# Kernel tuning notes

Hardware: AMD Instinct MI355X
Metric: run time of the kernel (lower is better)

The kernel has to match this reference:

```python
import jax, jax.numpy as jnp
import numpy as np

EMBED = 768
HEADS = 12
HEAD_DIM = EMBED // HEADS

def setup_inputs() -> dict:
    key = jax.random.key(0)
    k1, k2, k3, k4 = jax.random.split(key, 4)
    x = jax.random.normal(k1, (8, 1024, EMBED), dtype=jnp.float32)
    # qkv Linear (no bias per qkv_bias=False); proj Linear with bias
    w_qkv = jax.random.normal(k2, (EMBED, 3 * EMBED), dtype=jnp.float32) * 0.02
    w_proj = jax.random.normal(k3, (EMBED, EMBED), dtype=jnp.float32) * 0.02
    b_proj = jax.random.normal(k4, (EMBED,), dtype=jnp.float32) * 0.02
    return {"x": x, "w_qkv": w_qkv, "w_proj": w_proj, "b_proj": b_proj}

def reference(x, w_qkv, w_proj, b_proj):
    b, n, e = x.shape
    h, d = HEADS, HEAD_DIM
    scale = d ** (-0.5)
    qkv = x @ w_qkv                                    # [b, n, 3*e]
    qkv = qkv.reshape(b, n, 3, h, d)                   # (qkv h d) split order
    q, k, v = (jnp.transpose(qkv[:, :, i], (0, 2, 1, 3)) for i in range(3))  # [b,h,n,d]
    dots = jnp.einsum('bhid,bhjd->bhij', q, k) * scale
    attn = jax.nn.softmax(dots, axis=-1)               # dropout p=0 -> identity
    out = jnp.einsum('bhij,bhjd->bhid', attn, v)       # [b,h,n,d]
    out = jnp.transpose(out, (0, 2, 1, 3)).reshape(b, n, e)
    return out @ w_proj + b_proj
```

## Files before the change

kernel.cpp:

```cpp
#include <hip/hip_runtime.h>

typedef _Float16 f16;
typedef _Float16 half8 __attribute__((ext_vector_type(8)));
typedef _Float16 half4v __attribute__((ext_vector_type(4)));
typedef __fp16 fp16x2 __attribute__((ext_vector_type(2)));
typedef float f32x4 __attribute__((ext_vector_type(4)));
typedef float f32x16 __attribute__((ext_vector_type(16)));
typedef unsigned uint4v __attribute__((ext_vector_type(4)));

#define MFMA16(a,b,c) __builtin_amdgcn_mfma_f32_16x16x32_f16((a),(b),(c),0,0,0)
#define MFMA32(a,b,c) __builtin_amdgcn_mfma_f32_32x32x16_f16((a),(b),(c),0,0,0)

__device__ __forceinline__ void gload_lds16(const f16* g, f16* l) {
    __builtin_amdgcn_global_load_lds(
        (const __attribute__((address_space(1))) unsigned int*)g,
        (__attribute__((address_space(3))) unsigned int*)l, 16, 0, 0);
}

__device__ __forceinline__ void plswap(unsigned &a, unsigned &b) {
    asm volatile("v_permlane32_swap_b32 %0, %1" : "+v"(a), "+v"(b));
}

__device__ __forceinline__ unsigned pk2(float a, float b) {
    return __builtin_bit_cast(unsigned, __builtin_amdgcn_cvt_pkrtz(a, b));
}

__device__ __forceinline__ float fexp2(float x) {
#if __has_builtin(__builtin_amdgcn_exp2f)
    return __builtin_amdgcn_exp2f(x);
#else
    return exp2f(x);
#endif
}

__device__ __forceinline__ float xswap32(float x, int hi) {
    unsigned a = __builtin_bit_cast(unsigned, x), b = a;
    asm volatile("v_permlane32_swap_b32 %0, %1" : "+v"(a), "+v"(b));
    return __builtin_bit_cast(float, hi ? a : b);
}

__global__ void prep_kernel(const float* __restrict__ x, f16* __restrict__ x_h,
                            const float* __restrict__ w_qkv, f16* __restrict__ w_qkv_t,
                            const float* __restrict__ w_proj, f16* __restrict__ w_proj_t)
{
    __shared__ f16 tile[32][33];
    const int bidx = blockIdx.x;
    if (bidx < 6144) {
        int i = bidx * 256 + threadIdx.x;
        float4 v = ((const float4*)x)[i];
        half4v h;
        h.x = (f16)v.x; h.y = (f16)v.y; h.z = (f16)v.z; h.w = (f16)v.w;
        ((half4v*)x_h)[i] = h;
        return;
    }
    const float* in;  f16* out;  int N, idx;
    if (bidx < 6144 + 1728) { idx = bidx - 6144; in = w_qkv;  out = w_qkv_t;  N = 2304; }
    else                    { idx = bidx - 7872; in = w_proj; out = w_proj_t; N = 768;  }
    const int K = 768;
    int n0 = (idx % (N / 32)) * 32, k0 = (idx / (N / 32)) * 32;
    int tx = threadIdx.x & 31, ty = threadIdx.x >> 5;
    for (int r = ty; r < 32; r += 8)
        tile[r][tx] = (f16)in[(size_t)(k0 + r) * N + (n0 + tx)];
    __syncthreads();
    for (int r = ty; r < 32; r += 8)
        out[(size_t)(n0 + r) * K + (k0 + tx)] = tile[tx][r];
}

__global__ __launch_bounds__(256, 5)
void gemm_qkv(const f16* __restrict__ A, const f16* __restrict__ Bt,
              f16* __restrict__ qbuf, f16* __restrict__ kbuf, f16* __restrict__ vtbuf)
{
    constexpr int K = 768;
    constexpr int NX = 18;
    constexpr int NWG = NX * 64;
    __shared__ __align__(16) char smem[32768];
    f16* As = (f16*)smem;
    f16* Bs = (f16*)(smem + 16384);
    const int tid  = threadIdx.x;
    const int lane = tid & 63, wave = tid >> 6;
    const int wm = wave >> 1, wn = wave & 1;
    const int l15 = lane & 15, l4 = lane >> 4;

    const int bid = blockIdx.x;
    const int swz = (bid & 7) * (NWG / 8) + (bid >> 3);
    const int m0 = (swz / NX) * 128, n0 = (swz % NX) * 128;

    const int srow  = lane >> 2;
    const int sslot = lane & 3;

    f32x4 acc[4][4] = {};

    #define GSTAGE(buf, kt) do {                                                     \
        _Pragma("unroll")                                                            \
        for (int i = 0; i < 2; ++i) {                                                \
            int rbase = i * 64 + wave * 16;                                          \
            int row = rbase + srow;                                                  \
            gload_lds16(A  + (size_t)(m0 + row) * K + (kt) + sslot * 8, &As[(buf) * 4096 + rbase * 32]); \
            gload_lds16(Bt + (size_t)(n0 + row) * K + (kt) + sslot * 8, &Bs[(buf) * 4096 + rbase * 32]); \
        }                                                                            \
    } while (0)

    GSTAGE(0, 0);
    __syncthreads();

    for (int t = 0; t < 24; ++t) {
        const int cur = t & 1;
        if (t < 23) GSTAGE(cur ^ 1, (t + 1) * 32);
        half8 af[4], bf[4];
        #pragma unroll
        for (int mi = 0; mi < 4; mi++) af[mi] = *(const half8*)&As[cur*4096 + (wm*64 + mi*16 + l15) * 32 + l4*8];
        #pragma unroll
        for (int ni = 0; ni < 4; ni++) bf[ni] = *(const half8*)&Bs[cur*4096 + (wn*64 + ni*16 + l15) * 32 + l4*8];
        #pragma unroll
        for (int mi = 0; mi < 4; mi++)
            #pragma unroll
            for (int ni = 0; ni < 4; ni++)
                acc[mi][ni] = MFMA16(af[mi], bf[ni], acc[mi][ni]);
        __syncthreads();
    }
    #undef GSTAGE

    const int t3 = n0 / 768;
    const int bb = m0 >> 10;
    const int mo = m0 & 1023;
    const int h0 = (n0 - t3 * 768) >> 6;

    if (t3 < 2) {
        f16* sC = (f16*)smem;
        f16* outb = (t3 == 0) ? qbuf : kbuf;
        #pragma unroll
        for (int hh = 0; hh < 2; hh++) {
            if (wm == hh) {
                #pragma unroll
                for (int mi = 0; mi < 4; mi++)
                    #pragma unroll
                    for (int ni = 0; ni < 4; ni++)
                        #pragma unroll
                        for (int r = 0; r < 4; r++) {
                            int row = mi*16 + l4*4 + r;
                            int col = wn*64 + ni*16 + l15;
                            sC[row * 136 + col] = (f16)acc[mi][ni][r];
                        }
            }
            __syncthreads();
            #pragma unroll
            for (int hc = 0; hc < 2; hc++) {
                f16* base = outb + ((size_t)(bb * 12 + h0 + hc) * 1024 + mo + hh * 64) * 64;
                #pragma unroll
                for (int i = 0; i < 2; i++) {
                    int row = i * 32 + (tid >> 3);
                    int cc  = (tid & 7) * 8;
                    half8 v = *(const half8*)&sC[row * 136 + hc * 64 + cc];
                    *(half8*)(base + row * 64 + cc) = v;
                }
            }
            __syncthreads();
        }
    } else {
        f16* sC = (f16*)smem;
        #pragma unroll
        for (int hh = 0; hh < 2; hh++) {
            if (wn == hh) {
                #pragma unroll
                for (int mi = 0; mi < 4; mi++)
                    #pragma unroll
                    for (int ni = 0; ni < 4; ni++) {
                        int row0 = wm*64 + mi*16 + l4*4;
                        int col  = ni*16 + l15;
                        half4v pk;
                        #pragma unroll
                        for (int r = 0; r < 4; r++) pk[r] = (f16)acc[mi][ni][r];
                        *(half4v*)&sC[col * 136 + row0] = pk;
                    }
            }
            __syncthreads();
            #pragma unroll
            for (int i = 0; i < 4; i++) {
                int col = i * 16 + (tid >> 4);
                int rc  = (tid & 15) * 8;
                half8 v = *(const half8*)&sC[col * 136 + rc];
                int colg = hh * 64 + col;
                int head = h0 + (colg >> 6), dd = colg & 63;
                *(half8*)(vtbuf + ((size_t)(bb * 12 + head) * 64 + dd) * 1024 + mo + rc) = v;
            }
            __syncthreads();
        }
    }
}

__global__ __launch_bounds__(256, 3)
void gemm_proj(const f16* __restrict__ A, const f16* __restrict__ Bt,
               float* __restrict__ out, const float* __restrict__ bias)
{
    constexpr int K = 768;
    constexpr int NX = 6;
    constexpr int NWG = NX * 64;
    __shared__ __align__(16) char smem[49152];
    f16* As = (f16*)smem;
    f16* Bs = (f16*)(smem + 24576);
    const int tid  = threadIdx.x;
    const int lane = tid & 63, wave = tid >> 6;
    const int wm = wave >> 1, wn = wave & 1;
    const int l15 = lane & 15, l4 = lane >> 4;

    const int bid = blockIdx.x;
    const int swz = (bid & 7) * (NWG / 8) + (bid >> 3);
    const int m0 = (swz / NX) * 128, n0 = (swz % NX) * 128;

    const int srow  = lane >> 2;
    const int sslot = lane & 3;

    f32x4 acc[4][4] = {};

    #define GSTAGE(buf, kt) do {                                                     \
        _Pragma("unroll")                                                            \
        for (int i = 0; i < 2; ++i) {                                                \
            int rbase = i * 64 + wave * 16;                                          \
            int row = rbase + srow;                                                  \
            gload_lds16(A  + (size_t)(m0 + row) * K + (kt) + sslot * 8, &As[(buf) * 4096 + rbase * 32]); \
            gload_lds16(Bt + (size_t)(n0 + row) * K + (kt) + sslot * 8, &Bs[(buf) * 4096 + rbase * 32]); \
        }                                                                            \
    } while (0)

    GSTAGE(0, 0);
    GSTAGE(1, 32);

    int cur = 0;
    for (int t = 0; t < 24; ++t) {
        if (t < 23) asm volatile("s_waitcnt vmcnt(4)" ::: "memory");
        else        asm volatile("s_waitcnt vmcnt(0)" ::: "memory");
        __builtin_amdgcn_s_barrier();
        if (t < 22) {
            int nb = cur + 2; if (nb >= 3) nb -= 3;
            GSTAGE(nb, (t + 2) * 32);
        }
        half8 af[4], bf[4];
        #pragma unroll
        for (int mi = 0; mi < 4; mi++) af[mi] = *(const half8*)&As[cur*4096 + (wm*64 + mi*16 + l15) * 32 + l4*8];
        #pragma unroll
        for (int ni = 0; ni < 4; ni++) bf[ni] = *(const half8*)&Bs[cur*4096 + (wn*64 + ni*16 + l15) * 32 + l4*8];
        #pragma unroll
        for (int mi = 0; mi < 4; mi++)
            #pragma unroll
            for (int ni = 0; ni < 4; ni++)
                acc[mi][ni] = MFMA16(af[mi], bf[ni], acc[mi][ni]);
        if (++cur >= 3) cur = 0;
    }
    #undef GSTAGE

    #pragma unroll
    for (int mi = 0; mi < 4; mi++)
        #pragma unroll
        for (int ni = 0; ni < 4; ni++)
            #pragma unroll
            for (int r = 0; r < 4; r++) {
                int gm = m0 + wm*64 + mi*16 + l4*4 + r;
                int gn = n0 + wn*64 + ni*16 + l15;
                out[(size_t)gm * 768 + gn] = acc[mi][ni][r] + bias[gn];
            }
}

__global__ __launch_bounds__(256, 3)
void attn_kernel(const f16* __restrict__ qbuf, const f16* __restrict__ kbuf,
                 const f16* __restrict__ vtbuf, f16* __restrict__ obuf)
{
    __shared__ __align__(16) f16 Ks[3][4096];
    __shared__ __align__(16) f16 Vs[3][4096];
    const int tid = threadIdx.x;
    const int lane = tid & 63, wave = tid >> 6;
    const int bh = blockIdx.x;
    const int b = bh / 12, h = bh % 12;
    const int q0 = blockIdx.y * 128 + wave * 32;
    const int l31 = lane & 31, hi = lane >> 5;
    const int sw0 = (l31 & 7) << 4;

    const f16* Q  = qbuf  + (size_t)bh * 65536;
    const f16* Kp = kbuf  + (size_t)bh * 65536;
    const f16* Vt = vtbuf + (size_t)bh * 65536;

    const f16 slh = (f16)(0.125f * 1.44269504089f);
    half8 aq[4];
    #pragma unroll
    for (int c = 0; c < 4; c++) {
        aq[c] = *(const half8*)&Q[(size_t)(q0 + l31) * 64 + c * 16 + hi * 8];
        #pragma unroll
        for (int j = 0; j < 8; j++) aq[c][j] *= slh;
    }

    const int srow8 = lane >> 3;
    const int c16   = (lane & 7) ^ srow8;

    f32x16 o0 = {}, o1 = {};
    float lrq = 0.f, mrq = 0.f, stale = 0.f;

    #define STAGE(buf, kv) do {                                                     \
        _Pragma("unroll")                                                           \
        for (int i = 0; i < 2; ++i) {                                               \
            int rbase = wave * 16 + i * 8;                                          \
            int rl = rbase + srow8;                                                 \
            gload_lds16(Kp + (size_t)((kv) + rl) * 64 + c16 * 8, &Ks[buf][rbase * 64]); \
            gload_lds16(Vt + (size_t)rl * 1024 + (kv) + c16 * 8, &Vs[buf][rbase * 64]); \
        }                                                                           \
    } while (0)

    #define QKISSUE(dst0, dst1, kb, minit) do {                                     \
        _Pragma("unroll")                                                           \
        for (int j = 0; j < 16; j++) { dst0[j] = (minit); dst1[j] = (minit); }      \
        __builtin_amdgcn_s_setprio(1);                                              \
        _Pragma("unroll")                                                           \
        for (int c = 0; c < 4; c++) {                                               \
            int koff = (c * 32 + hi * 16) ^ sw0;                                    \
            half8 k0 = *(const half8*)((kb) + l31 * 128 + koff);                    \
            half8 k1 = *(const half8*)((kb) + (32 + l31) * 128 + koff);             \
            dst0 = MFMA32(k0, aq[c], dst0);                                         \
            dst1 = MFMA32(k1, aq[c], dst1);                                         \
        }                                                                           \
        __builtin_amdgcn_s_setprio(0);                                              \
    } while (0)

    STAGE(0, 0);
    STAGE(1, 64);
    __syncthreads();

    f32x16 st0, st1;
    QKISSUE(st0, st1, (const char*)&Ks[0][0], 0.f);

    int bcur = 0;
    for (int t = 0; t < 16; ++t) {
        int bn1 = bcur + 1; if (bn1 >= 3) bn1 -= 3;
        int bn2 = bcur + 2; if (bn2 >= 3) bn2 -= 3;

        if (t < 14) STAGE(bn2, (t + 2) * 64);

        f32x16 sN0, sN1;
        if (t < 15) QKISSUE(sN0, sN1, (const char*)&Ks[bn1][0], -mrq);

        if (__any(stale != 0.f)) {
            #pragma unroll
            for (int j = 0; j < 16; j++) { st0[j] -= stale; st1[j] -= stale; }
        }
        stale = 0.f;

        float m16;
        {
            float p0 = fmaxf(fmaxf(st0[0],  st0[1]),  fmaxf(st0[2],  st0[3]));
            float p1 = fmaxf(fmaxf(st0[4],  st0[5]),  fmaxf(st0[6],  st0[7]));
            float p2 = fmaxf(fmaxf(st0[8],  st0[9]),  fmaxf(st0[10], st0[11]));
            float p3 = fmaxf(fmaxf(st0[12], st0[13]), fmaxf(st0[14], st0[15]));
            float r0 = fmaxf(fmaxf(st1[0],  st1[1]),  fmaxf(st1[2],  st1[3]));
            float r1 = fmaxf(fmaxf(st1[4],  st1[5]),  fmaxf(st1[6],  st1[7]));
            float r2 = fmaxf(fmaxf(st1[8],  st1[9]),  fmaxf(st1[10], st1[11]));
            float r3 = fmaxf(fmaxf(st1[12], st1[13]), fmaxf(st1[14], st1[15]));
            m16 = fmaxf(fmaxf(fmaxf(p0, p1), fmaxf(p2, p3)),
                        fmaxf(fmaxf(r0, r1), fmaxf(r2, r3)));
        }
        m16 = fmaxf(m16, xswap32(m16, hi));

        if (!__all(m16 <= 11.0f)) {
            float d = fmaxf(m16, 0.f);
            float alpha = fexp2(-d);
            mrq += d;
            stale = d;
            #pragma unroll
            for (int j = 0; j < 16; j++) { st0[j] -= d; st1[j] -= d; }
            lrq *= alpha;
            #pragma unroll
            for (int reg = 0; reg < 16; reg++) {
                float a = __shfl(alpha, (reg & 3) + 8 * (reg >> 2) + 4 * hi);
                o0[reg] *= a; o1[reg] *= a;
            }
        }

        float rs = 0.f;
        half8 pa[4];
        #pragma unroll
        for (int tile = 0; tile < 2; tile++) {
            const f32x16& sv = tile ? st1 : st0;
            #pragma unroll
            for (int half16 = 0; half16 < 2; half16++) {
                int rb = half16 * 8;
                unsigned A1, B1, A2, B2;
                {
                    float e0 = fexp2(sv[rb+0]), e1 = fexp2(sv[rb+1]);
                    float e4 = fexp2(sv[rb+4]), e5 = fexp2(sv[rb+5]);
                    rs += (e0 + e1) + (e4 + e5);
                    A1 = pk2(e0, e1); B1 = pk2(e4, e5);
                    plswap(A1, B1);
                }
                {
                    float e2 = fexp2(sv[rb+2]), e3 = fexp2(sv[rb+3]);
                    float e6 = fexp2(sv[rb+6]), e7 = fexp2(sv[rb+7]);
                    rs += (e2 + e3) + (e6 + e7);
                    A2 = pk2(e2, e3); B2 = pk2(e6, e7);
                    plswap(A2, B2);
                }
                uint4v w = {A1, A2, B1, B2};
                pa[tile * 2 + half16] = __builtin_bit_cast(half8, w);
            }
        }
        rs += xswap32(rs, hi);
        lrq += rs;

        {
            const char* Vb = (const char*)&Vs[bcur][0];
            __builtin_amdgcn_s_setprio(1);
            #pragma unroll
            for (int kc = 0; kc < 4; kc++) {
                int koff = (kc * 32 + hi * 16) ^ sw0;
                half8 v0 = *(const half8*)(Vb + l31 * 128 + koff);
                half8 v1 = *(const half8*)(Vb + (32 + l31) * 128 + koff);
                o0 = MFMA32(pa[kc], v0, o0);
                o1 = MFMA32(pa[kc], v1, o1);
            }
            __builtin_amdgcn_s_setprio(0);
        }

        if (t < 15) {
            asm volatile("s_waitcnt vmcnt(0)" ::: "memory");
            __builtin_amdgcn_s_barrier();
            st0 = sN0; st1 = sN1;
        }
        bcur = bn1;
    }
    #undef QKISSUE
    #undef STAGE

    float rq = 1.0f / lrq;
    f16* Op = obuf + (size_t)b * 1024 * 768 + h * 64;
    #pragma unroll
    for (int reg = 0; reg < 16; reg++) {
        int qrow = (reg & 3) + 8 * (reg >> 2) + 4 * hi;
        float inv = __shfl(rq, qrow);
        size_t base = (size_t)(q0 + qrow) * 768;
        Op[base + l31]      = (f16)(o0[reg] * inv);
        Op[base + 32 + l31] = (f16)(o1[reg] * inv);
    }
}

extern "C" void kernel_launch(void* const* d_in, const int* in_sizes, int n_in,
                              void* d_out, int out_size, void* d_ws, size_t ws_size,
                              hipStream_t stream) {
    const float* x      = (const float*)d_in[0];
    const float* w_qkv  = (const float*)d_in[1];
    const float* w_proj = (const float*)d_in[2];
    const float* b_proj = (const float*)d_in[3];
    float* out = (float*)d_out;
    char* ws = (char*)d_ws;

    f16* x_h      = (f16*)(ws + 0);
    f16* w_qkv_t  = (f16*)(ws + 12582912);
    f16* w_proj_t = (f16*)(ws + 16121856);
    f16* qb       = (f16*)(ws + 17301504);
    f16* kb       = (f16*)(ws + 29884416);
    f16* vtb      = (f16*)(ws + 42467328);
    f16* ob       = (f16*)(ws + 55050240);

    prep_kernel<<<dim3(6144 + 1728 + 576), dim3(256), 0, stream>>>(
        x, x_h, w_qkv, w_qkv_t, w_proj, w_proj_t);
    gemm_qkv<<<dim3(18 * 64), dim3(256), 0, stream>>>(x_h, w_qkv_t, qb, kb, vtb);
    attn_kernel<<<dim3(96, 8), dim3(256), 0, stream>>>(qb, kb, vtb, ob);
    gemm_proj<<<dim3(6 * 64), dim3(256), 0, stream>>>(ob, w_proj_t, out, b_proj);
}
```

Measured before the change: 142.1 us.

## Triple-buffer QKV GEMM loads and stage full epilogue tile in one pass

The QKV GEMM main loop moves from double to triple buffering with async global-to-LDS loads issued two stages ahead, gated by explicit vmcnt waits and one barrier per iteration instead of two. The epilogue now writes the whole 128x128 tile into LDS at once, so each output path needs a single barrier-separated pass rather than two halves with extra syncs. LDS grows to 48 KB and the occupancy hint drops from 5 to 3 workgroups, which may reduce latency hiding across waves.

```diff
diff --git a/kernel.cpp b/kernel.cpp
--- a/kernel.cpp
+++ b/kernel.cpp
@@ -66,16 +66,16 @@
         out[(size_t)(n0 + r) * K + (k0 + tx)] = tile[tx][r];
 }
 
-__global__ __launch_bounds__(256, 5)
+__global__ __launch_bounds__(256, 3)
 void gemm_qkv(const f16* __restrict__ A, const f16* __restrict__ Bt,
               f16* __restrict__ qbuf, f16* __restrict__ kbuf, f16* __restrict__ vtbuf)
 {
     constexpr int K = 768;
     constexpr int NX = 18;
     constexpr int NWG = NX * 64;
-    __shared__ __align__(16) char smem[32768];
+    __shared__ __align__(16) char smem[49152];
     f16* As = (f16*)smem;
-    f16* Bs = (f16*)(smem + 16384);
+    f16* Bs = (f16*)(smem + 24576);
     const int tid  = threadIdx.x;
     const int lane = tid & 63, wave = tid >> 6;
     const int wm = wave >> 1, wn = wave & 1;
@@ -101,11 +101,17 @@
     } while (0)
 
     GSTAGE(0, 0);
-    __syncthreads();
-
+    GSTAGE(1, 32);
+
+    int cur = 0;
     for (int t = 0; t < 24; ++t) {
-        const int cur = t & 1;
-        if (t < 23) GSTAGE(cur ^ 1, (t + 1) * 32);
+        if (t < 23) asm volatile("s_waitcnt vmcnt(4)" ::: "memory");
+        else        asm volatile("s_waitcnt vmcnt(0)" ::: "memory");
+        __builtin_amdgcn_s_barrier();
+        if (t < 22) {
+            int nb = cur + 2; if (nb >= 3) nb -= 3;
+            GSTAGE(nb, (t + 2) * 32);
+        }
         half8 af[4], bf[4];
         #pragma unroll
         for (int mi = 0; mi < 4; mi++) af[mi] = *(const half8*)&As[cur*4096 + (wm*64 + mi*16 + l15) * 32 + l4*8];
@@ -116,74 +122,61 @@
             #pragma unroll
             for (int ni = 0; ni < 4; ni++)
                 acc[mi][ni] = MFMA16(af[mi], bf[ni], acc[mi][ni]);
-        __syncthreads();
+        if (++cur >= 3) cur = 0;
     }
     #undef GSTAGE
 
+    __syncthreads();
+    f16* sC = (f16*)smem;
     const int t3 = n0 / 768;
     const int bb = m0 >> 10;
     const int mo = m0 & 1023;
     const int h0 = (n0 - t3 * 768) >> 6;
 
     if (t3 < 2) {
-        f16* sC = (f16*)smem;
+        #pragma unroll
+        for (int mi = 0; mi < 4; mi++)
+            #pragma unroll
+            for (int ni = 0; ni < 4; ni++)
+                #pragma unroll
+                for (int r = 0; r < 4; r++) {
+                    int row = wm*64 + mi*16 + l4*4 + r;
+                    int col = wn*64 + ni*16 + l15;
+                    sC[row * 136 + col] = (f16)acc[mi][ni][r];
+                }
+        __syncthreads();
         f16* outb = (t3 == 0) ? qbuf : kbuf;
         #pragma unroll
-        for (int hh = 0; hh < 2; hh++) {
-            if (wm == hh) {
+        for (int hc = 0; hc < 2; hc++) {
+            f16* base = outb + ((size_t)(bb * 12 + h0 + hc) * 1024 + mo) * 64;
+            #pragma unroll
+            for (int i = 0; i < 4; i++) {
+                int row = wave * 32 + i * 8 + (lane >> 3);
+                int cc  = (lane & 7) * 8;
+                half8 v = *(const half8*)&sC[row * 136 + hc * 64 + cc];
+                *(half8*)(base + row * 64 + cc) = v;
+            }
+        }
+    } else {
+        #pragma unroll
+        for (int mi = 0; mi < 4; mi++)
+            #pragma unroll
+            for (int ni = 0; ni < 4; ni++) {
+                int row0 = wm*64 + mi*16 + l4*4;
+                int col  = wn*64 + ni*16 + l15;
+                half4v pk;
                 #pragma unroll
-                for (int mi = 0; mi < 4; mi++)
-                    #pragma unroll
-                    for (int ni = 0; ni < 4; ni++)
-                        #pragma unroll
-                        for (int r = 0; r < 4; r++) {
-                            int row = mi*16 + l4*4 + r;
-                            int col = wn*64 + ni*16 + l15;
-                            sC[row * 136 + col] = (f16)acc[mi][ni][r];
-                        }
-            }
-            __syncthreads();
-            #pragma unroll
-            for (int hc = 0; hc < 2; hc++) {
-                f16* base = outb + ((size_t)(bb * 12 + h0 + hc) * 1024 + mo + hh * 64) * 64;
-                #pragma unroll
-                for (int i = 0; i < 2; i++) {
-                    int row = i * 32 + (tid >> 3);
-                    int cc  = (tid & 7) * 8;
-                    half8 v = *(const half8*)&sC[row * 136 + hc * 64 + cc];
-                    *(half8*)(base + row * 64 + cc) = v;
-                }
-            }
-            __syncthreads();
-        }
-    } else {
-        f16* sC = (f16*)smem;
-        #pragma unroll
-        for (int hh = 0; hh < 2; hh++) {
-            if (wn == hh) {
-                #pragma unroll
-                for (int mi = 0; mi < 4; mi++)
-                    #pragma unroll
-                    for (int ni = 0; ni < 4; ni++) {
-                        int row0 = wm*64 + mi*16 + l4*4;
-                        int col  = ni*16 + l15;
-                        half4v pk;
-                        #pragma unroll
-                        for (int r = 0; r < 4; r++) pk[r] = (f16)acc[mi][ni][r];
-                        *(half4v*)&sC[col * 136 + row0] = pk;
-                    }
-            }
-            __syncthreads();
-            #pragma unroll
-            for (int i = 0; i < 4; i++) {
-                int col = i * 16 + (tid >> 4);
-                int rc  = (tid & 15) * 8;
-                half8 v = *(const half8*)&sC[col * 136 + rc];
-                int colg = hh * 64 + col;
-                int head = h0 + (colg >> 6), dd = colg & 63;
-                *(half8*)(vtbuf + ((size_t)(bb * 12 + head) * 64 + dd) * 1024 + mo + rc) = v;
-            }
-            __syncthreads();
+                for (int r = 0; r < 4; r++) pk[r] = (f16)acc[mi][ni][r];
+                *(half4v*)&sC[col * 136 + row0] = pk;
+            }
+        __syncthreads();
+        #pragma unroll
+        for (int i = 0; i < 8; i++) {
+            int col = wave * 32 + i * 4 + (lane >> 4);
+            int rc  = (lane & 15) * 8;
+            half8 v = *(const half8*)&sC[col * 136 + rc];
+            int head = h0 + (col >> 6), dd = col & 63;
+            *(half8*)(vtbuf + ((size_t)(bb * 12 + head) * 64 + dd) * 1024 + mo + rc) = v;
         }
     }
 }
```

Result: faster. 118.0 us (-17.0%).
